# Optimization experiments

Measured on AMD Instinct MI355X. Metric: run time of the kernel, lower is better.

The kernel has to match this reference:

```python
import jax, jax.numpy as jnp
import numpy as np
import math

D = 256; B = 4; N = 2048; IN = 16; POS = 3; LAT = 128
DEPTH = 3; RATIO = 0.5; NBLK = 8  # depth*2 + 2 final blocks


def _silu(x):
    return x * jax.nn.sigmoid(x)


def _ln(h, g, b):
    m = h.mean(-1, keepdims=True)
    v = h.var(-1, keepdims=True)  # biased, matches nn.LayerNorm
    return (h - m) / jnp.sqrt(v + 1e-5) * g + b


def _block(h, A, g, b, w1, b1, w2, b2, eps):
    # h: (B, n, D), A: (B, n, n) binary adjacency (block-diag equivalent)
    hn = _ln(h, g, b)
    nb = jnp.einsum('bij,bjd->bid', A, hn)  # sparse.mm(adj, h) per graph
    t = (1.0 + eps) * hn + nb
    t = _silu(t @ w1 + b1) @ w2 + b2
    return h + t


def _forward(x, adj, pos, in_w, in_b, pw1, pb1, pw2, pb2,
             bg, bb, bw1, bb1, bw2, bb2, beps, pool_p, lw, lb, batch_size):
    Bsz = batch_size
    n = adj.shape[0]
    d = in_w.shape[1]
    h = x @ in_w + in_b  # (B*N, D)
    # positional embedding: tile, normalize (unbiased std like torch), MLP
    pt = jnp.tile(pos, (Bsz, 1))
    pn = (pt - pt.mean(0, keepdims=True)) / (pt.std(0, ddof=1, keepdims=True) + 1e-8)
    pe = _silu(pn @ pw1 + pb1) @ pw2 + pb2
    h = (h + pe).reshape(Bsz, n, d)
    A = jnp.broadcast_to(adj, (Bsz, n, n))  # shared block-diag tiles
    blk = 0
    for dep in range(DEPTH):
        for _ in range(2):  # blocks_per_stage
            h = _block(h, A, bg[blk], bb[blk], bw1[blk], bb1[blk],
                       bw2[blk], bb2[blk], beps[blk])
            blk += 1
        # TopKPool: projection score, per-graph top-k, tanh gating
        p = pool_p[dep]
        score = h @ p / jnp.linalg.norm(p)  # (B, n)
        k = int(math.ceil(RATIO * h.shape[1]))  # static
        idx = jnp.sort(jax.lax.top_k(score, k)[1], axis=-1)  # (B, k)
        gate = jnp.tanh(jnp.take_along_axis(score, idx, axis=1))
        h = jnp.take_along_axis(h, idx[:, :, None], axis=1) * gate[:, :, None]
        # subgraph_coo + to_binary: adj[idx][:, idx] per graph
        A = jax.vmap(lambda a, i: a[i][:, i])(A, idx)
        A = (A > 0).astype(h.dtype)
    for _ in range(2):  # final_stage
        h = _block(h, A, bg[blk], bb[blk], bw1[blk], bb1[blk],
                   bw2[blk], bb2[blk], beps[blk])
        blk += 1
    hm = h.mean(1)
    hs = h.std(1, ddof=1) + 1e-6  # torch .std is unbiased
    return jnp.concatenate([hm, hs], axis=-1) @ lw + lb  # (B, LAT)


def setup_inputs() -> dict:
    key = jax.random.key(0)
    ks = jax.random.split(key, 12)
    f32 = jnp.float32
    s = 1.0 / np.sqrt(D)
    x = jax.random.normal(ks[0], (B * N, IN), f32)
    adj = (jax.random.uniform(ks[1], (N, N)) < 0.004).astype(f32)  # ~8 nbrs/node
    pos = jax.random.normal(ks[2], (N, POS), f32)
    return {
        'x': x, 'adj': adj, 'pos': pos,
        'in_w': jax.random.normal(ks[3], (IN, D), f32) / np.sqrt(IN),
        'in_b': jnp.zeros(D, f32),
        'pw1': jax.random.normal(ks[4], (POS, D), f32) / np.sqrt(POS),
        'pb1': jnp.zeros(D, f32),
        'pw2': jax.random.normal(ks[5], (D, D), f32) * s,
        'pb2': jnp.zeros(D, f32),
        'bg': jnp.ones((NBLK, D), f32),
        'bb': jnp.zeros((NBLK, D), f32),
        'bw1': jax.random.normal(ks[6], (NBLK, D, D), f32) * s,
        'bb1': jnp.zeros((NBLK, D), f32),
        'bw2': jax.random.normal(ks[7], (NBLK, D, D), f32) * (0.5 * s),
        'bb2': jnp.zeros((NBLK, D), f32),
        'beps': jnp.zeros(NBLK, f32),
        'pool_p': jax.random.normal(ks[8], (DEPTH, D), f32) * s,
        'lw': jax.random.normal(ks[9], (2 * D, LAT), f32) / np.sqrt(2 * D),
        'lb': jnp.zeros(LAT, f32),
        'batch_size': B,
    }


def reference(x, adj, pos, in_w, in_b, pw1, pb1, pw2, pb2,
              bg, bb, bw1, bb1, bw2, bb2, beps, pool_p, lw, lb, batch_size):
    return _forward(x, adj, pos, in_w, in_b, pw1, pb1, pw2, pb2,
                    bg, bb, bw1, bb1, bw2, bb2, beps, pool_p, lw, lb, batch_size)
```

## Files before the change

### kernel.cpp

```cpp
#include <hip/hip_runtime.h>
#include <hip/hip_bf16.h>

#define NTOT 2048
#define DD 256
#define BSZ 4

typedef _Float16 half_t;
typedef __attribute__((ext_vector_type(8))) _Float16 halfx8;
typedef __attribute__((ext_vector_type(4))) _Float16 halfx4;
typedef __attribute__((ext_vector_type(4))) float f32x4;

__device__ __forceinline__ f32x4 h2f(halfx4 v) {
    f32x4 r;
#pragma unroll
    for (int e = 0; e < 4; ++e) r[e] = (float)v[e];
    return r;
}
__device__ __forceinline__ halfx4 f2h(f32x4 v) {
    halfx4 r;
#pragma unroll
    for (int e = 0; e < 4; ++e) r[e] = (half_t)v[e];
    return r;
}

__device__ __forceinline__ float blockReduceSum256(float v) {
    __shared__ float red[4];
    for (int off = 32; off > 0; off >>= 1) v += __shfl_down(v, off);
    int lane = threadIdx.x & 63, w = threadIdx.x >> 6;
    __syncthreads();
    if (lane == 0) red[w] = v;
    __syncthreads();
    return red[0] + red[1] + red[2] + red[3];
}

__device__ __forceinline__ int blockScan256(int v, int* wsum) {
    int lane = threadIdx.x & 63, w = threadIdx.x >> 6;
#pragma unroll
    for (int off = 1; off < 64; off <<= 1) {
        int t = __shfl_up(v, off);
        if (lane >= off) v += t;
    }
    __syncthreads();
    if (lane == 63) wsum[w] = v;
    __syncthreads();
    int add = 0;
#pragma unroll
    for (int i = 0; i < 4; ++i) add += (i < w) ? wsum[i] : 0;
    return v + add;
}

#define SB_WPREP 4352
#define SB_STAT  4356
#define SB_A2L   4868
#define SB_MAPS  4900
__global__ void __launch_bounds__(256) setup_kernel(
    const float* __restrict__ bw1, const float* __restrict__ bw2,
    const float* __restrict__ pw2, half_t* __restrict__ Wt,
    const float* __restrict__ pos, float* __restrict__ pstats,
    const float* __restrict__ poolp, float* __restrict__ pinv,
    const float* __restrict__ adj, int* __restrict__ ldeg0, int* __restrict__ lcol0,
    int* __restrict__ orig, int* __restrict__ inv) {
    int bid = blockIdx.x, tid = threadIdx.x;
    if (bid < SB_WPREP) {
        int m = bid >> 8, rem = bid & 255;
        int nb = (rem >> 4) * 16, kb = (rem & 15) * 16;
        const float* W = (m < 8) ? (bw1 + (size_t)m * DD * DD)
                      : (m < 16) ? (bw2 + (size_t)(m - 8) * DD * DD)
                                 : pw2;
        __shared__ float s[16][17];
        int i = tid >> 4, j = tid & 15;
        s[i][j] = W[(size_t)(kb + i) * DD + nb + j];
        __syncthreads();
        Wt[(size_t)m * DD * DD + (size_t)(nb + i) * DD + kb + j] = (half_t)s[j][i];
    } else if (bid < SB_STAT) {
        int which = bid - SB_WPREP;
        if (which == 0) {
            float s[3] = {0.f, 0.f, 0.f};
            for (int i = tid; i < NTOT; i += 256)
                for (int c = 0; c < 3; ++c) s[c] += pos[i * 3 + c];
            float m[3];
            for (int c = 0; c < 3; ++c) m[c] = blockReduceSum256(s[c]) / (float)NTOT;
            float q[3] = {0.f, 0.f, 0.f};
            for (int i = tid; i < NTOT; i += 256)
                for (int c = 0; c < 3; ++c) { float d = pos[i * 3 + c] - m[c]; q[c] += d * d; }
            for (int c = 0; c < 3; ++c) {
                float t = blockReduceSum256(q[c]);
                if (tid == 0) {
                    float var = ((float)BSZ * t) / ((float)BSZ * NTOT - 1.0f);
                    pstats[c] = m[c];
                    pstats[3 + c] = 1.0f / (sqrtf(var) + 1e-8f);
                }
            }
        } else {
            int dep = which - 1;
            float v = poolp[dep * DD + tid];
            float ss = blockReduceSum256(v * v);
            if (tid == 0) pinv[dep] = rsqrtf(ss);
        }
    } else if (bid < SB_A2L) {
        int row = (bid - SB_STAT) * 4 + (tid >> 6);
        int lane = tid & 63;
        int run = 0;
        for (int j0 = 0; j0 < NTOT; j0 += 64) {
            int j = j0 + lane;
            bool pred = adj[(size_t)row * NTOT + j] != 0.f;
            unsigned long long mask = __ballot(pred);
            if (pred) {
                int pos2 = run + __popcll(mask & ((1ull << lane) - 1ull));
                if (pos2 < 64) lcol0[row * 64 + pos2] = j;
            }
            run += __popcll(mask);
        }
        if (lane == 0) ldeg0[row] = run < 64 ? run : 64;
    } else {
        int t = (bid - SB_A2L) * 256 + tid;
        int i = t & (NTOT - 1);
        orig[t] = i; inv[t] = i;
    }
}

__global__ void __launch_bounds__(256) pe_h_kernel(
    const float* __restrict__ pos, const float* __restrict__ pstats,
    const float* __restrict__ pw1, const float* __restrict__ pb1,
    const half_t* __restrict__ Wt16, const float* __restrict__ pb2,
    const float* __restrict__ x, const float* __restrict__ in_w,
    const float* __restrict__ in_b, float* __restrict__ h, half_t* __restrict__ z) {
    __shared__ half_t tb[16][264];
    __shared__ float iw[16][DD];
    __shared__ float xs[16][16];
    __shared__ float part[4][16][2];
    __shared__ float mrs[16][2];
    int tid = threadIdx.x;
    int i0 = blockIdx.x * 16;
    {
        int rl = tid >> 4, cb = (tid & 15) * 16;
        float pn[3];
#pragma unroll
        for (int c = 0; c < 3; ++c)
            pn[c] = (pos[(i0 + rl) * 3 + c] - pstats[c]) * pstats[3 + c];
#pragma unroll
        for (int u = 0; u < 16; ++u) {
            int d = cb + u;
            float a = pb1[d];
            a += pn[0] * pw1[d];
            a += pn[1] * pw1[DD + d];
            a += pn[2] * pw1[2 * DD + d];
            a = a / (1.0f + expf(-a));
            tb[rl][d] = (half_t)a;
        }
        int k = tid >> 4;
#pragma unroll
        for (int u = 0; u < 16; ++u) iw[k][cb + u] = in_w[k * DD + cb + u];
    }
    __syncthreads();
    int w = tid >> 6, l = tid & 63;
    int lo = l & 15, hi = l >> 4;
    int kb = hi * 8;
    float pe_r[4][4];
    {
        f32x4 acc[4] = {};
#pragma unroll
        for (int k0 = 0; k0 < DD; k0 += 32) {
            halfx8 a0 = *(const halfx8*)&tb[lo][kb + k0];
#pragma unroll
            for (int j = 0; j < 4; ++j) {
                halfx8 bj = *(const halfx8*)(Wt16 + (size_t)(w * 64 + j * 16 + lo) * DD + kb + k0);
                acc[j] = __builtin_amdgcn_mfma_f32_16x16x32_f16(a0, bj, acc[j], 0, 0, 0);
            }
        }
#pragma unroll
        for (int j = 0; j < 4; ++j) {
            float bs = pb2[w * 64 + j * 16 + lo];
#pragma unroll
            for (int q = 0; q < 4; ++q) pe_r[j][q] = acc[j][q] + bs;
        }
    }
    float xb[4];
#pragma unroll
    for (int j = 0; j < 4; ++j) xb[j] = in_b[w * 64 + j * 16 + lo];
    for (int b = 0; b < BSZ; ++b) {
        __syncthreads();
        xs[tid >> 4][tid & 15] = x[(size_t)(b * NTOT + i0 + (tid >> 4)) * 16 + (tid & 15)];
        __syncthreads();
        float vh[4][4];
#pragma unroll
        for (int q = 0; q < 4; ++q) {
            int rl = hi * 4 + q;
            float s = 0.f, ss = 0.f;
#pragma unroll
            for (int j = 0; j < 4; ++j) {
                int c = w * 64 + j * 16 + lo;
                float acc = xb[j];
#pragma unroll
                for (int k = 0; k < 16; ++k) acc += xs[rl][k] * iw[k][c];
                float v = acc + pe_r[j][q];
                vh[j][q] = v;
                s += v; ss += v * v;
            }
#pragma unroll
            for (int m = 1; m < 16; m <<= 1) { s += __shfl_xor(s, m); ss += __shfl_xor(ss, m); }
            if (lo == 0) { part[w][rl][0] = s; part[w][rl][1] = ss; }
        }
        __syncthreads();
        if (tid < 16) {
            float s = 0.f, ss = 0.f;
#pragma unroll
            for (int w2 = 0; w2 < 4; ++w2) { s += part[w2][tid][0]; ss += part[w2][tid][1]; }
            float mean = s * (1.0f / DD);
            float var = ss * (1.0f / DD) - mean * mean;
            mrs[tid][0] = mean;
            mrs[tid][1] = rsqrtf(var + 1e-5f);
        }
        __syncthreads();
#pragma unroll
        for (int q = 0; q < 4; ++q) {
            int rl = hi * 4 + q;
            size_t r = (size_t)(b * NTOT + i0 + rl);
            float mean = mrs[rl][0], rs = mrs[rl][1];
#pragma unroll
            for (int j = 0; j < 4; ++j) {
                int c = w * 64 + j * 16 + lo;
                float v = vh[j][q];
                h[r * DD + c] = v;
                z[r * DD + c] = (half_t)((v - mean) * rs);
            }
        }
    }
}

template <int NWAVES, int SCORE>
__global__ void __launch_bounds__(NWAVES * 64) layer_kernel(
    float* __restrict__ h, const half_t* __restrict__ zin, half_t* __restrict__ zout,
    const half_t* __restrict__ Wt1, const half_t* __restrict__ Wt2,
    const float* __restrict__ b1v, const float* __restrict__ b2v,
    const float* __restrict__ gv, const float* __restrict__ bbv,
    const float* __restrict__ beps, int blk,
    const int* __restrict__ ldeg0, const int* __restrict__ lcol0,
    const int* __restrict__ orig, const int* __restrict__ inv,
    const float* __restrict__ poolp, const float* __restrict__ pinv_all,
    float* __restrict__ scores, int dep, int n, int tag) {
    constexpr int W = 256 / NWAVES;
    constexpr int JL = W / 16;
    constexpr int TPR = (NWAVES * 64) / 16;
    constexpr int CH = 64 / TPR;
    __shared__ half_t tb[16][264];
    __shared__ half_t ub[16][264];
    __shared__ float part[NWAVES][16][3];
    __shared__ float mrs[16][2];
    int tid = threadIdx.x;
    int bid = blockIdx.x;
    int xcd = bid & 7;
    int batch = xcd >> 1;
    int within = ((bid >> 3) << 1) | (xcd & 1);
    int rowBase = batch * n + within * 16;
    float eps1 = 1.0f + beps[blk];

    {
        int rl = tid / TPR, cg = tid % TPR;
        int r = rowBase + rl;
        int b = r / n, i = r - b * n;
        const halfx4* zb = (const halfx4*)zin + (size_t)b * n * 64;
        f32x4 acc[CH];
#pragma unroll
        for (int u = 0; u < CH; ++u) acc[u] = h2f(zb[(size_t)i * 64 + cg + TPR * u]) * eps1;
        int cnt = 0;
        if (tag == 0) {
            int deg = ldeg0[i];
            const int* lc = lcol0 + i * 64;
            int p = 0;
            for (; p + 4 <= deg; p += 4) {
                int j0 = lc[p], j1 = lc[p + 1], j2 = lc[p + 2], j3 = lc[p + 3];
#pragma unroll
                for (int u = 0; u < CH; ++u) {
                    f32x4 v0 = h2f(zb[(size_t)j0 * 64 + cg + TPR * u]);
                    f32x4 v1 = h2f(zb[(size_t)j1 * 64 + cg + TPR * u]);
                    f32x4 v2 = h2f(zb[(size_t)j2 * 64 + cg + TPR * u]);
                    f32x4 v3 = h2f(zb[(size_t)j3 * 64 + cg + TPR * u]);
                    acc[u] += (v0 + v1) + (v2 + v3);
                }
            }
            for (; p < deg; ++p) {
                int j = lc[p];
#pragma unroll
                for (int u = 0; u < CH; ++u) acc[u] += h2f(zb[(size_t)j * 64 + cg + TPR * u]);
            }
            cnt = deg;
        } else {
            int o = orig[b * NTOT + i];
            int deg = ldeg0[o];
            const int* lc = lcol0 + o * 64;
            const int* invb = inv + b * NTOT;
            int p = 0;
            for (; p + 4 <= deg; p += 4) {
                int v0 = invb[lc[p]], v1 = invb[lc[p + 1]];
                int v2 = invb[lc[p + 2]], v3 = invb[lc[p + 3]];
                if ((v0 >> 12) == tag) {
                    int j = v0 & 4095; ++cnt;
#pragma unroll
                    for (int u = 0; u < CH; ++u) acc[u] += h2f(zb[(size_t)j * 64 + cg + TPR * u]);
                }
                if ((v1 >> 12) == tag) {
                    int j = v1 & 4095; ++cnt;
#pragma unroll
                    for (int u = 0; u < CH; ++u) acc[u] += h2f(zb[(size_t)j * 64 + cg + TPR * u]);
                }
                if ((v2 >> 12) == tag) {
                    int j = v2 & 4095; ++cnt;
#pragma unroll
                    for (int u = 0; u < CH; ++u) acc[u] += h2f(zb[(size_t)j * 64 + cg + TPR * u]);
                }
                if ((v3 >> 12) == tag) {
                    int j = v3 & 4095; ++cnt;
#pragma unroll
                    for (int u = 0; u < CH; ++u) acc[u] += h2f(zb[(size_t)j * 64 + cg + TPR * u]);
                }
            }
            for (; p < deg; ++p) {
                int v = invb[lc[p]];
                if ((v >> 12) == tag) {
                    int j = v & 4095; ++cnt;
#pragma unroll
                    for (int u = 0; u < CH; ++u) acc[u] += h2f(zb[(size_t)j * 64 + cg + TPR * u]);
                }
            }
        }
        float coefb = eps1 + (float)cnt;
#pragma unroll
        for (int u = 0; u < CH; ++u) {
            int c4 = cg + TPR * u;
            f32x4 gvv = ((const f32x4*)gv)[c4];
            f32x4 bvv = ((const f32x4*)bbv)[c4];
            f32x4 tv = gvv * acc[u] + bvv * coefb;
            *(halfx4*)&tb[rl][c4 * 4] = f2h(tv);
        }
    }
    __syncthreads();

    int w = tid >> 6, l = tid & 63;
    int lo = l & 15, hi = l >> 4;
    int kb = hi * 8;

    {
        f32x4 acc[JL] = {};
#pragma unroll
        for (int k0 = 0; k0 < DD; k0 += 32) {
            halfx8 a0 = *(const halfx8*)&tb[lo][kb + k0];
#pragma unroll
            for (int j = 0; j < JL; ++j) {
                halfx8 bj = *(const halfx8*)(Wt1 + (size_t)(w * W + j * 16 + lo) * DD + kb + k0);
                acc[j] = __builtin_amdgcn_mfma_f32_16x16x32_f16(a0, bj, acc[j], 0, 0, 0);
            }
        }
        float bs[JL];
#pragma unroll
        for (int j = 0; j < JL; ++j) bs[j] = b1v[w * W + j * 16 + lo];
#pragma unroll
        for (int q = 0; q < 4; ++q)
#pragma unroll
            for (int j = 0; j < JL; ++j) {
                float v = acc[j][q] + bs[j];
                v = v / (1.0f + expf(-v));
                ub[hi * 4 + q][w * W + j * 16 + lo] = (half_t)v;
            }
    }
    __syncthreads();

    {
        f32x4 acc[JL] = {};
#pragma unroll
        for (int k0 = 0; k0 < DD; k0 += 32) {
            halfx8 a0 = *(const halfx8*)&ub[lo][kb + k0];
#pragma unroll
            for (int j = 0; j < JL; ++j) {
                halfx8 bj = *(const halfx8*)(Wt2 + (size_t)(w * W + j * 16 + lo) * DD + kb + k0);
                acc[j] = __builtin_amdgcn_mfma_f32_16x16x32_f16(a0, bj, acc[j], 0, 0, 0);
            }
        }
        float bs[JL], pv[JL];
#pragma unroll
        for (int j = 0; j < JL; ++j) { bs[j] = b2v[w * W + j * 16 + lo]; pv[j] = 0.f; }
        if (SCORE) {
#pragma unroll
            for (int j = 0; j < JL; ++j) pv[j] = poolp[dep * DD + w * W + j * 16 + lo];
        }
        float vh[JL][4];
#pragma unroll
        for (int q = 0; q < 4; ++q) {
            int r = rowBase + hi * 4 + q;
            float s = 0.f, ss = 0.f, sp = 0.f;
#pragma unroll
            for (int j = 0; j < JL; ++j) {
                int c = w * W + j * 16 + lo;
                float v = h[(size_t)r * DD + c] + acc[j][q] + bs[j];
                vh[j][q] = v;
                s += v; ss += v * v;
                if (SCORE) sp += v * pv[j];
            }
#pragma unroll
            for (int m = 1; m < 16; m <<= 1) {
                s += __shfl_xor(s, m); ss += __shfl_xor(ss, m);
                if (SCORE) sp += __shfl_xor(sp, m);
            }
            if (lo == 0) {
                int rl = hi * 4 + q;
                part[w][rl][0] = s; part[w][rl][1] = ss;
                if (SCORE) part[w][rl][2] = sp;
            }
        }
        __syncthreads();
        if (tid < 16) {
            float s = 0.f, ss = 0.f, sp = 0.f;
#pragma unroll
            for (int w2 = 0; w2 < NWAVES; ++w2) {
                s += part[w2][tid][0]; ss += part[w2][tid][1];
                if (SCORE) sp += part[w2][tid][2];
            }
            float mean = s * (1.0f / DD);
            float var = ss * (1.0f / DD) - mean * mean;
            mrs[tid][0] = mean;
            mrs[tid][1] = rsqrtf(var + 1e-5f);
            if (SCORE) {
                int r = rowBase + tid;
                int b2 = r / n, ii = r - b2 * n;
                scores[b2 * NTOT + ii] = sp * pinv_all[dep];
            }
        }
        __syncthreads();
#pragma unroll
        for (int q = 0; q < 4; ++q) {
            int rl = hi * 4 + q;
            int r = rowBase + rl;
            float mean = mrs[rl][0], rs = mrs[rl][1];
#pragma unroll
            for (int j = 0; j < JL; ++j) {
                int c = w * W + j * 16 + lo;
                float v = vh[j][q];
                h[(size_t)r * DD + c] = v;
                zout[(size_t)r * DD + c] = (half_t)((v - mean) * rs);
            }
        }
    }
}

__global__ void topk_kernel(const float* __restrict__ scores, const int* __restrict__ orig_cur,
                            int* __restrict__ orig_next, int* __restrict__ idx_local,
                            float* __restrict__ gate, int n, int k) {
    __shared__ unsigned keys[2048];
    __shared__ int hist[256];
    __shared__ int wsum[4];
    __shared__ int sh_bucket, sh_r, sh_cnt, sh_tot;
    __shared__ unsigned cand[256];
    __shared__ unsigned sh_thr;
    int b = blockIdx.x;
    const float* sc = scores + b * NTOT;
    int tid = threadIdx.x;
    for (int i = tid; i < n; i += 256) {
        unsigned u = __float_as_uint(sc[i]);
        keys[i] = (u & 0x80000000u) ? ~u : (u | 0x80000000u);
    }
    hist[tid] = 0;
    if (tid == 0) sh_cnt = 0;
    __syncthreads();
    for (int i = tid; i < n; i += 256) atomicAdd(&hist[keys[i] >> 24], 1);
    __syncthreads();
    int cnt = hist[tid];
    int incl = blockScan256(cnt, wsum);
    int r = n - k;
    int excl = incl - cnt;
    if (excl <= r && r < incl) { sh_bucket = tid; sh_r = r - excl; }
    __syncthreads();
    int b1 = sh_bucket, r1 = sh_r;
    int c = hist[b1];
    unsigned thrkey;
    if (c <= 256) {
        for (int i = tid; i < n; i += 256) {
            unsigned key = keys[i];
            if ((key >> 24) == (unsigned)b1) {
                int pos = atomicAdd(&sh_cnt, 1);
                cand[pos] = key;
            }
        }
        __syncthreads();
        if (tid < c) {
            unsigned mine = cand[tid];
            int less = 0, eq = 0;
            for (int j = 0; j < c; ++j) {
                unsigned oth = cand[j];
                less += (oth < mine); eq += (oth == mine);
            }
            if (less <= r1 && r1 < less + eq) sh_thr = mine;
        }
        __syncthreads();
        thrkey = sh_thr;
    } else {
        unsigned prefix = ((unsigned)b1) << 24;
        int rr = r1;
        for (int shift = 16; shift >= 0; shift -= 8) {
            __syncthreads();
            hist[tid] = 0;
            __syncthreads();
            unsigned mask = 0xFFFFFFFFu << (shift + 8);
            for (int i = tid; i < n; i += 256) {
                unsigned key = keys[i];
                if ((key & mask) == (prefix & mask)) atomicAdd(&hist[(key >> shift) & 255], 1);
            }
            __syncthreads();
            int cnt2 = hist[tid];
            int incl2 = blockScan256(cnt2, wsum);
            int excl2 = incl2 - cnt2;
            if (excl2 <= rr && rr < incl2) { sh_bucket = tid; sh_r = rr - excl2; }
            __syncthreads();
            prefix |= ((unsigned)sh_bucket) << shift;
            rr = sh_r;
            __syncthreads();
        }
        thrkey = prefix;
    }
    unsigned uthr = (thrkey & 0x80000000u) ? (thrkey ^ 0x80000000u) : ~thrkey;
    float thr = __uint_as_float(uthr);
    int chunk = n / 256;
    int base = tid * chunk;
    int cgt = 0, ceq = 0;
    for (int u = 0; u < chunk; ++u) {
        float s = sc[base + u];
        cgt += (s > thr); ceq += (s == thr);
    }
    int packed = (cgt << 12) | ceq;
    int pincl = blockScan256(packed, wsum);
    if (tid == 255) sh_tot = pincl;
    __syncthreads();
    int total_gt = sh_tot >> 12;
    int ties = k - total_gt;
    int pexcl = pincl - packed;
    int gtb = pexcl >> 12, eqb = pexcl & 4095;
    for (int u = 0; u < chunk; ++u) {
        int i = base + u;
        float s = sc[i];
        bool isgt = (s > thr), iseq = (s == thr);
        bool keep = isgt || (iseq && eqb < ties);
        if (keep) {
            int pos = gtb + (eqb < ties ? eqb : ties);
            idx_local[b * NTOT + pos] = i;
            gate[b * NTOT + pos] = tanhf(s);
            orig_next[b * NTOT + pos] = orig_cur[b * NTOT + i];
        }
        gtb += isgt; eqb += iseq;
    }
}

__global__ void __launch_bounds__(64) gather_kernel(
    const float* __restrict__ h, const int* __restrict__ idx_local,
    const float* __restrict__ gate, const int* __restrict__ orig_new,
    float* __restrict__ hout, half_t* __restrict__ zout, int* __restrict__ inv,
    int n_old, int k, int tag) {
    int bid = blockIdx.x;
    int xcd = bid & 7;
    int b = xcd >> 1;
    int rr = ((bid >> 3) << 1) | (xcd & 1);
    int r = b * k + rr;
    int lane = threadIdx.x;
    int src = idx_local[b * NTOT + rr];
    float gg = gate[b * NTOT + rr];
    f32x4 v = ((const f32x4*)h)[(size_t)(b * n_old + src) * 64 + lane] * gg;
    ((f32x4*)hout)[(size_t)r * 64 + lane] = v;
    float s = v[0] + v[1] + v[2] + v[3];
    float ss = v[0] * v[0] + v[1] * v[1] + v[2] * v[2] + v[3] * v[3];
#pragma unroll
    for (int m = 1; m < 64; m <<= 1) { s += __shfl_xor(s, m); ss += __shfl_xor(ss, m); }
    float mean = s * (1.0f / DD);
    float rs = rsqrtf(ss * (1.0f / DD) - mean * mean + 1e-5f);
    ((halfx4*)zout)[(size_t)r * 64 + lane] = f2h((v - mean) * rs);
    if (lane == 0) inv[b * NTOT + orig_new[b * NTOT + rr]] = (tag << 12) | rr;
}

__global__ void __launch_bounds__(256) readout_final_kernel(
    const float* __restrict__ h, const float* __restrict__ lw,
    const float* __restrict__ lb, float* __restrict__ out) {
    __shared__ float feat[512];
    int b = blockIdx.x, d = threadIdx.x;
    const float* hb = h + (size_t)b * 256 * DD;
    float s = 0.f;
    for (int i = 0; i < 256; ++i) s += hb[(size_t)i * DD + d];
    float mean = s / 256.0f;
    float s2 = 0.f;
    for (int i = 0; i < 256; ++i) {
        float diff = hb[(size_t)i * DD + d] - mean;
        s2 += diff * diff;
    }
    feat[d] = mean;
    feat[256 + d] = sqrtf(s2 / 255.0f) + 1e-6f;
    __syncthreads();
    if (d < 128) {
        float acc = lb[d];
        for (int k = 0; k < 512; ++k) acc += feat[k] * lw[k * 128 + d];
        out[b * 128 + d] = acc;
    }
}

extern "C" void kernel_launch(void* const* d_in, const int* in_sizes, int n_in,
                              void* d_out, int out_size, void* d_ws, size_t ws_size,
                              hipStream_t stream) {
    (void)in_sizes; (void)n_in; (void)out_size; (void)ws_size;
    const float* x     = (const float*)d_in[0];
    const float* adj   = (const float*)d_in[1];
    const float* pos   = (const float*)d_in[2];
    const float* in_w  = (const float*)d_in[3];
    const float* in_b  = (const float*)d_in[4];
    const float* pw1   = (const float*)d_in[5];
    const float* pb1   = (const float*)d_in[6];
    const float* pw2   = (const float*)d_in[7];
    const float* pb2   = (const float*)d_in[8];
    const float* bg    = (const float*)d_in[9];
    const float* bb    = (const float*)d_in[10];
    const float* bw1   = (const float*)d_in[11];
    const float* bb1   = (const float*)d_in[12];
    const float* bw2   = (const float*)d_in[13];
    const float* bb2   = (const float*)d_in[14];
    const float* beps  = (const float*)d_in[15];
    const float* poolp = (const float*)d_in[16];
    const float* lw    = (const float*)d_in[17];
    const float* lb    = (const float*)d_in[18];
    float* out = (float*)d_out;

    char* wp = (char*)d_ws;
    auto alloc = [&](size_t bytes) -> void* {
        void* p = (void*)wp;
        wp += (bytes + 255) & ~(size_t)255;
        return p;
    };
    const size_t HBYTES = (size_t)BSZ * NTOT * DD * sizeof(float);
    float*  h    = (float*)alloc(HBYTES);
    float*  bufC = (float*)alloc(HBYTES);
    half_t* zA   = (half_t*)alloc(HBYTES / 2);
    half_t* zB   = (half_t*)alloc(HBYTES / 2);
    half_t* Wt   = (half_t*)alloc((size_t)17 * DD * DD * sizeof(half_t));
    float* pstats  = (float*)alloc(8 * sizeof(float));
    float* pinv    = (float*)alloc(4 * sizeof(float));
    float* scores  = (float*)alloc(BSZ * NTOT * sizeof(float));
    float* gate    = (float*)alloc(BSZ * NTOT * sizeof(float));
    int*   origA   = (int*)alloc(BSZ * NTOT * sizeof(int));
    int*   origB   = (int*)alloc(BSZ * NTOT * sizeof(int));
    int*   idxl    = (int*)alloc(BSZ * NTOT * sizeof(int));
    int*   inv     = (int*)alloc(BSZ * NTOT * sizeof(int));
    int*   ldeg0   = (int*)alloc(NTOT * sizeof(int));
    int*   lcol0   = (int*)alloc((size_t)NTOT * 64 * sizeof(int));

    setup_kernel<<<SB_MAPS, 256, 0, stream>>>(bw1, bw2, pw2, Wt, pos, pstats, poolp, pinv,
                                              adj, ldeg0, lcol0, origA, inv);
    pe_h_kernel<<<NTOT / 16, 256, 0, stream>>>(pos, pstats, pw1, pb1,
                                               Wt + (size_t)16 * DD * DD, pb2,
                                               x, in_w, in_b, h, zA);

    float* hcur = h;
    float* halt = bufC;
    half_t* zin = zA;
    half_t* zout = zB;
    int* orig = origA;
    int* orign = origB;
    int n = NTOT;
    int blk = 0;
    for (int dep = 0; dep < 4; ++dep) {
        for (int s = 0; s < 2; ++s) {
            int rows = BSZ * n;
            const half_t* W1 = Wt + (size_t)blk * DD * DD;
            const half_t* W2 = Wt + (size_t)(8 + blk) * DD * DD;
            const float* B1 = bb1 + blk * DD;
            const float* B2 = bb2 + blk * DD;
            const float* G  = bg + blk * DD;
            const float* BB = bb + blk * DD;
            int sc = (s == 1 && dep < 3) ? 1 : 0;
            if (dep < 2) {
                if (sc) layer_kernel<16, 1><<<rows / 16, 1024, 0, stream>>>(
                    hcur, zin, zout, W1, W2, B1, B2, G, BB, beps, blk,
                    ldeg0, lcol0, orig, inv, poolp, pinv, scores, dep, n, dep);
                else    layer_kernel<16, 0><<<rows / 16, 1024, 0, stream>>>(
                    hcur, zin, zout, W1, W2, B1, B2, G, BB, beps, blk,
                    ldeg0, lcol0, orig, inv, nullptr, nullptr, nullptr, 0, n, dep);
            } else {
                if (sc) layer_kernel<8, 1><<<rows / 16, 512, 0, stream>>>(
                    hcur, zin, zout, W1, W2, B1, B2, G, BB, beps, blk,
                    ldeg0, lcol0, orig, inv, poolp, pinv, scores, dep, n, dep);
                else    layer_kernel<8, 0><<<rows / 16, 512, 0, stream>>>(
                    hcur, zin, zout, W1, W2, B1, B2, G, BB, beps, blk,
                    ldeg0, lcol0, orig, inv, nullptr, nullptr, nullptr, 0, n, dep);
            }
            { half_t* t = zin; zin = zout; zout = t; }
            ++blk;
        }
        if (dep < 3) {
            int k = n / 2;
            topk_kernel<<<BSZ, 256, 0, stream>>>(scores, orig, orign, idxl, gate, n, k);
            { int* t = orig; orig = orign; orign = t; }
            gather_kernel<<<BSZ * k, 64, 0, stream>>>(hcur, idxl, gate, orig, halt, zin, inv,
                                                      n, k, dep + 1);
            { float* t = hcur; hcur = halt; halt = t; }
            n = k;
        }
    }
    readout_final_kernel<<<BSZ, 256, 0, stream>>>(hcur, lw, lb, out);
}
```

Measured before the change: 255.9 us.

## Use 16-wave layer kernel at all depths and parallelize readout across blocks

Removes the NWAVES template so every layer launch uses 1024 threads (16 waves, one 16-column MFMA tile each), including the deeper stages that previously used 8 waves. The final readout is split into a 32-block column-parallel statistics kernel plus a small linear kernel, replacing a 4-block serial loop over rows. This trades extra launch overhead and a one-pass variance formula, which is less numerically stable, for more parallelism in the tail.

```diff
diff --git a/kernel.cpp b/kernel.cpp
--- a/kernel.cpp
+++ b/kernel.cpp
@@ -228,8 +228,8 @@
     }
 }
 
-template <int NWAVES, int SCORE>
-__global__ void __launch_bounds__(NWAVES * 64) layer_kernel(
+template <int SCORE>
+__global__ void __launch_bounds__(1024) layer_kernel(
     float* __restrict__ h, const half_t* __restrict__ zin, half_t* __restrict__ zout,
     const half_t* __restrict__ Wt1, const half_t* __restrict__ Wt2,
     const float* __restrict__ b1v, const float* __restrict__ b2v,
@@ -239,13 +239,9 @@
     const int* __restrict__ orig, const int* __restrict__ inv,
     const float* __restrict__ poolp, const float* __restrict__ pinv_all,
     float* __restrict__ scores, int dep, int n, int tag) {
-    constexpr int W = 256 / NWAVES;
-    constexpr int JL = W / 16;
-    constexpr int TPR = (NWAVES * 64) / 16;
-    constexpr int CH = 64 / TPR;
     __shared__ half_t tb[16][264];
     __shared__ half_t ub[16][264];
-    __shared__ float part[NWAVES][16][3];
+    __shared__ float part[16][16][3];
     __shared__ float mrs[16][2];
     int tid = threadIdx.x;
     int bid = blockIdx.x;
@@ -256,13 +252,11 @@
     float eps1 = 1.0f + beps[blk];
 
     {
-        int rl = tid / TPR, cg = tid % TPR;
+        int rl = tid >> 6, cg = tid & 63;
         int r = rowBase + rl;
         int b = r / n, i = r - b * n;
         const halfx4* zb = (const halfx4*)zin + (size_t)b * n * 64;
-        f32x4 acc[CH];
-#pragma unroll
-        for (int u = 0; u < CH; ++u) acc[u] = h2f(zb[(size_t)i * 64 + cg + TPR * u]) * eps1;
+        f32x4 acc = h2f(zb[(size_t)i * 64 + cg]) * eps1;
         int cnt = 0;
         if (tag == 0) {
             int deg = ldeg0[i];
@@ -270,20 +264,13 @@
             int p = 0;
             for (; p + 4 <= deg; p += 4) {
                 int j0 = lc[p], j1 = lc[p + 1], j2 = lc[p + 2], j3 = lc[p + 3];
-#pragma unroll
-                for (int u = 0; u < CH; ++u) {
-                    f32x4 v0 = h2f(zb[(size_t)j0 * 64 + cg + TPR * u]);
-                    f32x4 v1 = h2f(zb[(size_t)j1 * 64 + cg + TPR * u]);
-                    f32x4 v2 = h2f(zb[(size_t)j2 * 64 + cg + TPR * u]);
-                    f32x4 v3 = h2f(zb[(size_t)j3 * 64 + cg + TPR * u]);
-                    acc[u] += (v0 + v1) + (v2 + v3);
-                }
-            }
-            for (; p < deg; ++p) {
-                int j = lc[p];
-#pragma unroll
-                for (int u = 0; u < CH; ++u) acc[u] += h2f(zb[(size_t)j * 64 + cg + TPR * u]);
-            }
+                f32x4 v0 = h2f(zb[(size_t)j0 * 64 + cg]);
+                f32x4 v1 = h2f(zb[(size_t)j1 * 64 + cg]);
+                f32x4 v2 = h2f(zb[(size_t)j2 * 64 + cg]);
+                f32x4 v3 = h2f(zb[(size_t)j3 * 64 + cg]);
+                acc += (v0 + v1) + (v2 + v3);
+            }
+            for (; p < deg; ++p) acc += h2f(zb[(size_t)lc[p] * 64 + cg]);
             cnt = deg;
         } else {
             int o = orig[b * NTOT + i];
@@ -294,45 +281,21 @@
             for (; p + 4 <= deg; p += 4) {
                 int v0 = invb[lc[p]], v1 = invb[lc[p + 1]];
                 int v2 = invb[lc[p + 2]], v3 = invb[lc[p + 3]];
-                if ((v0 >> 12) == tag) {
-                    int j = v0 & 4095; ++cnt;
-#pragma unroll
-                    for (int u = 0; u < CH; ++u) acc[u] += h2f(zb[(size_t)j * 64 + cg + TPR * u]);
-                }
-                if ((v1 >> 12) == tag) {
-                    int j = v1 & 4095; ++cnt;
-#pragma unroll
-                    for (int u = 0; u < CH; ++u) acc[u] += h2f(zb[(size_t)j * 64 + cg + TPR * u]);
-                }
-                if ((v2 >> 12) == tag) {
-                    int j = v2 & 4095; ++cnt;
-#pragma unroll
-                    for (int u = 0; u < CH; ++u) acc[u] += h2f(zb[(size_t)j * 64 + cg + TPR * u]);
-                }
-                if ((v3 >> 12) == tag) {
-                    int j = v3 & 4095; ++cnt;
-#pragma unroll
-                    for (int u = 0; u < CH; ++u) acc[u] += h2f(zb[(size_t)j * 64 + cg + TPR * u]);
-                }
+                if ((v0 >> 12) == tag) { acc += h2f(zb[(size_t)(v0 & 4095) * 64 + cg]); ++cnt; }
+                if ((v1 >> 12) == tag) { acc += h2f(zb[(size_t)(v1 & 4095) * 64 + cg]); ++cnt; }
+                if ((v2 >> 12) == tag) { acc += h2f(zb[(size_t)(v2 & 4095) * 64 + cg]); ++cnt; }
+                if ((v3 >> 12) == tag) { acc += h2f(zb[(size_t)(v3 & 4095) * 64 + cg]); ++cnt; }
             }
             for (; p < deg; ++p) {
                 int v = invb[lc[p]];
-                if ((v >> 12) == tag) {
-                    int j = v & 4095; ++cnt;
-#pragma unroll
-                    for (int u = 0; u < CH; ++u) acc[u] += h2f(zb[(size_t)j * 64 + cg + TPR * u]);
-                }
+                if ((v >> 12) == tag) { acc += h2f(zb[(size_t)(v & 4095) * 64 + cg]); ++cnt; }
             }
         }
         float coefb = eps1 + (float)cnt;
-#pragma unroll
-        for (int u = 0; u < CH; ++u) {
-            int c4 = cg + TPR * u;
-            f32x4 gvv = ((const f32x4*)gv)[c4];
-            f32x4 bvv = ((const f32x4*)bbv)[c4];
-            f32x4 tv = gvv * acc[u] + bvv * coefb;
-            *(halfx4*)&tb[rl][c4 * 4] = f2h(tv);
-        }
+        f32x4 gvv = ((const f32x4*)gv)[cg];
+        f32x4 bvv = ((const f32x4*)bbv)[cg];
+        f32x4 tv = gvv * acc + bvv * coefb;
+        *(halfx4*)&tb[rl][cg * 4] = f2h(tv);
     }
     __syncthreads();
 
@@ -341,61 +304,42 @@
     int kb = hi * 8;
 
     {
-        f32x4 acc[JL] = {};
+        f32x4 acc = {};
 #pragma unroll
         for (int k0 = 0; k0 < DD; k0 += 32) {
             halfx8 a0 = *(const halfx8*)&tb[lo][kb + k0];
-#pragma unroll
-            for (int j = 0; j < JL; ++j) {
-                halfx8 bj = *(const halfx8*)(Wt1 + (size_t)(w * W + j * 16 + lo) * DD + kb + k0);
-                acc[j] = __builtin_amdgcn_mfma_f32_16x16x32_f16(a0, bj, acc[j], 0, 0, 0);
-            }
-        }
-        float bs[JL];
-#pragma unroll
-        for (int j = 0; j < JL; ++j) bs[j] = b1v[w * W + j * 16 + lo];
-#pragma unroll
-        for (int q = 0; q < 4; ++q)
-#pragma unroll
-            for (int j = 0; j < JL; ++j) {
-                float v = acc[j][q] + bs[j];
-                v = v / (1.0f + expf(-v));
-                ub[hi * 4 + q][w * W + j * 16 + lo] = (half_t)v;
-            }
+            halfx8 bj = *(const halfx8*)(Wt1 + (size_t)(w * 16 + lo) * DD + kb + k0);
+            acc = __builtin_amdgcn_mfma_f32_16x16x32_f16(a0, bj, acc, 0, 0, 0);
+        }
+        float bs = b1v[w * 16 + lo];
+#pragma unroll
+        for (int q = 0; q < 4; ++q) {
+            float v = acc[q] + bs;
+            v = v / (1.0f + expf(-v));
+            ub[hi * 4 + q][w * 16 + lo] = (half_t)v;
+        }
     }
     __syncthreads();
 
     {
-        f32x4 acc[JL] = {};
+        f32x4 acc = {};
 #pragma unroll
         for (int k0 = 0; k0 < DD; k0 += 32) {
             halfx8 a0 = *(const halfx8*)&ub[lo][kb + k0];
-#pragma unroll
-            for (int j = 0; j < JL; ++j) {
-                halfx8 bj = *(const halfx8*)(Wt2 + (size_t)(w * W + j * 16 + lo) * DD + kb + k0);
-                acc[j] = __builtin_amdgcn_mfma_f32_16x16x32_f16(a0, bj, acc[j], 0, 0, 0);
-            }
-        }
-        float bs[JL], pv[JL];
-#pragma unroll
-        for (int j = 0; j < JL; ++j) { bs[j] = b2v[w * W + j * 16 + lo]; pv[j] = 0.f; }
-        if (SCORE) {
-#pragma unroll
-            for (int j = 0; j < JL; ++j) pv[j] = poolp[dep * DD + w * W + j * 16 + lo];
-        }
-        float vh[JL][4];
+            halfx8 bj = *(const halfx8*)(Wt2 + (size_t)(w * 16 + lo) * DD + kb + k0);
+            acc = __builtin_amdgcn_mfma_f32_16x16x32_f16(a0, bj, acc, 0, 0, 0);
+        }
+        float bs = b2v[w * 16 + lo];
+        float pv = 0.f;
+        if (SCORE) pv = poolp[dep * DD + w * 16 + lo];
+        float vh[4];
 #pragma unroll
         for (int q = 0; q < 4; ++q) {
             int r = rowBase + hi * 4 + q;
-            float s = 0.f, ss = 0.f, sp = 0.f;
-#pragma unroll
-            for (int j = 0; j < JL; ++j) {
-                int c = w * W + j * 16 + lo;
-                float v = h[(size_t)r * DD + c] + acc[j][q] + bs[j];
-                vh[j][q] = v;
-                s += v; ss += v * v;
-                if (SCORE) sp += v * pv[j];
-            }
+            int c = w * 16 + lo;
+            float v = h[(size_t)r * DD + c] + acc[q] + bs;
+            vh[q] = v;
+            float s = v, ss = v * v, sp = SCORE ? v * pv : 0.f;
 #pragma unroll
             for (int m = 1; m < 16; m <<= 1) {
                 s += __shfl_xor(s, m); ss += __shfl_xor(ss, m);
@@ -411,7 +355,7 @@
         if (tid < 16) {
             float s = 0.f, ss = 0.f, sp = 0.f;
 #pragma unroll
-            for (int w2 = 0; w2 < NWAVES; ++w2) {
+            for (int w2 = 0; w2 < 16; ++w2) {
                 s += part[w2][tid][0]; ss += part[w2][tid][1];
                 if (SCORE) sp += part[w2][tid][2];
             }
@@ -431,13 +375,10 @@
             int rl = hi * 4 + q;
             int r = rowBase + rl;
             float mean = mrs[rl][0], rs = mrs[rl][1];
-#pragma unroll
-            for (int j = 0; j < JL; ++j) {
-                int c = w * W + j * 16 + lo;
-                float v = vh[j][q];
-                h[(size_t)r * DD + c] = v;
-                zout[(size_t)r * DD + c] = (half_t)((v - mean) * rs);
-            }
+            int c = w * 16 + lo;
+            float v = vh[q];
+            h[(size_t)r * DD + c] = v;
+            zout[(size_t)r * DD + c] = (half_t)((v - mean) * rs);
         }
     }
 }
@@ -573,28 +514,38 @@
     if (lane == 0) inv[b * NTOT + orig_new[b * NTOT + rr]] = (tag << 12) | rr;
 }
 
-__global__ void __launch_bounds__(256) readout_final_kernel(
-    const float* __restrict__ h, const float* __restrict__ lw,
-    const float* __restrict__ lb, float* __restrict__ out) {
-    __shared__ float feat[512];
-    int b = blockIdx.x, d = threadIdx.x;
-    const float* hb = h + (size_t)b * 256 * DD;
-    float s = 0.f;
-    for (int i = 0; i < 256; ++i) s += hb[(size_t)i * DD + d];
-    float mean = s / 256.0f;
-    float s2 = 0.f;
-    for (int i = 0; i < 256; ++i) {
-        float diff = hb[(size_t)i * DD + d] - mean;
-        s2 += diff * diff;
-    }
-    feat[d] = mean;
-    feat[256 + d] = sqrtf(s2 / 255.0f) + 1e-6f;
-    __syncthreads();
-    if (d < 128) {
-        float acc = lb[d];
-        for (int k = 0; k < 512; ++k) acc += feat[k] * lw[k * 128 + d];
-        out[b * 128 + d] = acc;
-    }
+__global__ void __launch_bounds__(256) readout_kernel(
+    const float* __restrict__ h, float* __restrict__ feat) {
+    __shared__ float red[8][32][2];
+    int bid = blockIdx.x;
+    int b = bid >> 3, dc = (bid & 7) * 32;
+    int cl = threadIdx.x & 31, rg = threadIdx.x >> 5;
+    const float* hb = h + (size_t)b * 256 * DD + dc + cl;
+    float s = 0.f, ss = 0.f;
+    for (int i = rg * 32; i < rg * 32 + 32; ++i) {
+        float v = hb[(size_t)i * DD];
+        s += v; ss += v * v;
+    }
+    red[rg][cl][0] = s; red[rg][cl][1] = ss;
+    __syncthreads();
+    if (rg == 0) {
+        float ts = 0.f, tss = 0.f;
+#pragma unroll
+        for (int j = 0; j < 8; ++j) { ts += red[j][cl][0]; tss += red[j][cl][1]; }
+        float mean = ts / 256.0f;
+        float s2 = tss - 256.0f * mean * mean;
+        feat[b * 512 + dc + cl] = mean;
+        feat[b * 512 + 256 + dc + cl] = sqrtf(fmaxf(s2, 0.f) / 255.0f) + 1e-6f;
+    }
+}
+
+__global__ void final_kernel(const float* __restrict__ feat, const float* __restrict__ lw,
+                             const float* __restrict__ lb, float* __restrict__ out) {
+    int b = blockIdx.x, l = threadIdx.x;
+    float acc = lb[l];
+    const float* f = feat + b * 512;
+    for (int k = 0; k < 512; ++k) acc += f[k] * lw[k * 128 + l];
+    out[b * 128 + l] = acc;
 }
 
 extern "C" void kernel_launch(void* const* d_in, const int* in_sizes, int n_in,
@@ -644,6 +595,7 @@
     int*   inv     = (int*)alloc(BSZ * NTOT * sizeof(int));
     int*   ldeg0   = (int*)alloc(NTOT * sizeof(int));
     int*   lcol0   = (int*)alloc((size_t)NTOT * 64 * sizeof(int));
+    float* feat    = (float*)alloc(BSZ * 512 * sizeof(float));
 
     setup_kernel<<<SB_MAPS, 256, 0, stream>>>(bw1, bw2, pw2, Wt, pos, pstats, poolp, pinv,
                                               adj, ldeg0, lcol0, origA, inv);
@@ -669,21 +621,12 @@
             const float* G  = bg + blk * DD;
             const float* BB = bb + blk * DD;
             int sc = (s == 1 && dep < 3) ? 1 : 0;
-            if (dep < 2) {
-                if (sc) layer_kernel<16, 1><<<rows / 16, 1024, 0, stream>>>(
-                    hcur, zin, zout, W1, W2, B1, B2, G, BB, beps, blk,
-                    ldeg0, lcol0, orig, inv, poolp, pinv, scores, dep, n, dep);
-                else    layer_kernel<16, 0><<<rows / 16, 1024, 0, stream>>>(
-                    hcur, zin, zout, W1, W2, B1, B2, G, BB, beps, blk,
-                    ldeg0, lcol0, orig, inv, nullptr, nullptr, nullptr, 0, n, dep);
-            } else {
-                if (sc) layer_kernel<8, 1><<<rows / 16, 512, 0, stream>>>(
-                    hcur, zin, zout, W1, W2, B1, B2, G, BB, beps, blk,
-                    ldeg0, lcol0, orig, inv, poolp, pinv, scores, dep, n, dep);
-                else    layer_kernel<8, 0><<<rows / 16, 512, 0, stream>>>(
-                    hcur, zin, zout, W1, W2, B1, B2, G, BB, beps, blk,
-                    ldeg0, lcol0, orig, inv, nullptr, nullptr, nullptr, 0, n, dep);
-            }
+            if (sc) layer_kernel<1><<<rows / 16, 1024, 0, stream>>>(
+                hcur, zin, zout, W1, W2, B1, B2, G, BB, beps, blk,
+                ldeg0, lcol0, orig, inv, poolp, pinv, scores, dep, n, dep);
+            else    layer_kernel<0><<<rows / 16, 1024, 0, stream>>>(
+                hcur, zin, zout, W1, W2, B1, B2, G, BB, beps, blk,
+                ldeg0, lcol0, orig, inv, nullptr, nullptr, nullptr, 0, n, dep);
             { half_t* t = zin; zin = zout; zout = t; }
             ++blk;
         }
@@ -697,5 +640,6 @@
             n = k;
         }
     }
-    readout_final_kernel<<<BSZ, 256, 0, stream>>>(hcur, lw, lb, out);
-}
+    readout_kernel<<<BSZ * 8, 256, 0, stream>>>(hcur, feat);
+    final_kernel<<<BSZ, 128, 0, stream>>>(feat, lw, lb, out);
+}
```

New measurement: 246.6 us. 1.04x faster.
